# Kernel tuning notes

Hardware: AMD Instinct MI355X
Metric: run time of the kernel (lower is better)

## Reference

```python
import jax, jax.numpy as jnp
import numpy as np

E, K, H, I = 64, 8, 2048, 768  # num_experts, top_k, hidden, moe_intermediate

def setup_inputs() -> dict:
    key = jax.random.key(0)
    k1, k2, k3, k4 = jax.random.split(key, 4)
    return {
        "hidden_states": jax.random.normal(k1, (1, 1024, H), dtype=jnp.float32),
        "w_gate": jax.random.normal(k2, (H, E), dtype=jnp.float32) * 0.02,
        "w13": jax.random.normal(k3, (E, H, 2 * I), dtype=jnp.float32) * 0.02,  # fused gate+up proj
        "w2": jax.random.normal(k4, (E, I, H), dtype=jnp.float32) * 0.02,
    }

def reference(hidden_states, w_gate, w13, w2):
    orig_shape = hidden_states.shape
    x = hidden_states.reshape(-1, orig_shape[-1])            # [T, H]
    T = x.shape[0]

    # Router: logits -> softmax -> top-k -> renormalize (norm_topk_prob=True)
    router_logits = x @ w_gate                               # [T, E]
    probs = jax.nn.softmax(router_logits, axis=-1)
    topk_w, topk_idx = jax.lax.top_k(probs, K)               # [T, K]
    topk_w = topk_w / jnp.sum(topk_w, axis=-1, keepdims=True)
    # Dense combine-weight matrix [T, E] (zero for non-routed experts)
    combine = jnp.zeros((T, E), dtype=x.dtype).at[
        jnp.arange(T)[:, None], topk_idx].add(topk_w)

    # Expert SwiGLU FFN, computed densely for all experts, masked by combine
    h = jnp.einsum('th,ehd->etd', x, w13)                    # [E, T, 2I]
    gate, up = h[..., :I], h[..., I:]
    act = jax.nn.silu(gate) * up                             # [E, T, I]
    y = jnp.einsum('eti,eih->eth', act, w2)                  # [E, T, H]
    out = jnp.einsum('eth,te->th', y, combine)               # [T, H]
    return out.reshape(orig_shape)
```

## Files before the change

kernel.cpp:

```cpp
#include <hip/hip_runtime.h>
#include <hip/hip_bf16.h>
#include <math.h>

#define NE 64
#define NK 8
#define NH 2048
#define NI 768
#define NT 1024

typedef float f32x4 __attribute__((ext_vector_type(4)));
typedef __bf16 bf16x8 __attribute__((ext_vector_type(8)));
typedef __bf16 bf16x4 __attribute__((ext_vector_type(4)));

__global__ __launch_bounds__(256) void router_k(
    const float* __restrict__ x, const float* __restrict__ wg,
    __bf16* __restrict__ x_bf, int* __restrict__ topk_idx,
    float* __restrict__ topk_w, int* __restrict__ counts)
{
    __shared__ float xs[4][NH];
    const int wave = threadIdx.x >> 6;
    const int lane = threadIdx.x & 63;
    const int t = blockIdx.x * 4 + wave;

    const float* xrow = x + (size_t)t * NH;
    __bf16* brow = x_bf + (size_t)t * NH;
    #pragma unroll
    for (int j = 0; j < 8; ++j) {
        int idx = j * 256 + lane * 4;
        f32x4 v = *reinterpret_cast<const f32x4*>(xrow + idx);
        *reinterpret_cast<f32x4*>(&xs[wave][idx]) = v;
        bf16x4 b;
        b[0] = (__bf16)v.x; b[1] = (__bf16)v.y; b[2] = (__bf16)v.z; b[3] = (__bf16)v.w;
        *reinterpret_cast<bf16x4*>(brow + idx) = b;
    }
    __syncthreads();

    float a0 = 0.f, a1 = 0.f, a2 = 0.f, a3 = 0.f;
    for (int h = 0; h < NH; h += 4) {
        a0 = fmaf(xs[wave][h + 0], wg[(h + 0) * NE + lane], a0);
        a1 = fmaf(xs[wave][h + 1], wg[(h + 1) * NE + lane], a1);
        a2 = fmaf(xs[wave][h + 2], wg[(h + 2) * NE + lane], a2);
        a3 = fmaf(xs[wave][h + 3], wg[(h + 3) * NE + lane], a3);
    }
    float acc = (a0 + a1) + (a2 + a3);

    float cur = acc;
    float sel_v[NK]; int sel_i[NK];
    #pragma unroll
    for (int k = 0; k < NK; ++k) {
        float bv = cur; int bi = lane;
        #pragma unroll
        for (int s = 32; s; s >>= 1) {
            float ov = __shfl_xor(bv, s, 64);
            int   oi = __shfl_xor(bi, s, 64);
            if (ov > bv || (ov == bv && oi < bi)) { bv = ov; bi = oi; }
        }
        sel_v[k] = bv; sel_i[k] = bi;
        if (lane == bi) cur = -3.4e38f;
    }
    float m = sel_v[0];
    float ssum = 0.f;
    #pragma unroll
    for (int k = 0; k < NK; ++k) ssum += expf(sel_v[k] - m);

    if (lane < NK) {
        float w = expf(sel_v[lane] - m) / ssum;
        topk_idx[t * NK + lane] = sel_i[lane];
        topk_w[t * NK + lane] = w;
        atomicAdd(&counts[sel_i[lane]], 1);
    }
}

__global__ void scan_k(const int* __restrict__ counts, int* __restrict__ offs,
                       int* __restrict__ cursors)
{
    if (threadIdx.x == 0) {
        int r = 0;
        for (int e = 0; e < NE; ++e) { offs[e] = r; r += counts[e]; }
        offs[NE] = r;
    }
    if (threadIdx.x < NE) cursors[threadIdx.x] = 0;
}

__global__ __launch_bounds__(256) void scatter_k(
    const int* __restrict__ topk_idx, const float* __restrict__ topk_w,
    const int* __restrict__ offs, int* __restrict__ cursors,
    int* __restrict__ slot_tok, float* __restrict__ slot_w,
    int* __restrict__ slot_of)
{
    int i = blockIdx.x * 256 + threadIdx.x;
    int e = topk_idx[i];
    int p = atomicAdd(&cursors[e], 1);
    int g = offs[e] + p;
    slot_tok[g] = i >> 3;
    slot_w[g] = topk_w[i];
    slot_of[i] = g;
}

__device__ __forceinline__ int swz(int row, int ch) { return ch ^ ((row >> 1) & 3); }

__global__ __launch_bounds__(256, 2) void e1_k(
    const __bf16* __restrict__ x_bf, const float* __restrict__ w13,
    const int* __restrict__ counts, const int* __restrict__ offs,
    const int* __restrict__ slot_tok, __bf16* __restrict__ act)
{
    const int e = blockIdx.x;
    const int cnt = counts[e];
    const int m0 = blockIdx.z * 256;
    if (m0 >= cnt) return;
    const int rows = min(256, cnt - m0);
    const int n0 = blockIdx.y * 64;
    const int goff = offs[e] + m0;

    __shared__ __bf16 A[2][256 * 32];
    __shared__ __bf16 B[2][128 * 32];
    __shared__ int tok[256];

    const int tid = threadIdx.x;
    tok[tid] = (tid < rows) ? slot_tok[goff + tid] : 0;
    __syncthreads();

    const int wave = tid >> 6, lane = tid & 63;
    f32x4 acc[4][8];
    #pragma unroll
    for (int i = 0; i < 4; ++i)
        #pragma unroll
        for (int j = 0; j < 8; ++j) acc[i][j] = (f32x4){0.f, 0.f, 0.f, 0.f};

    const float* w13e = w13 + (size_t)e * NH * (2 * NI);
    const int cc = tid & 31, kch = tid >> 5;
    const int bcol0 = cc * 4;
    const int gcol = (bcol0 < 64) ? (n0 + bcol0) : (NI + n0 + bcol0 - 64);

    const __bf16* aptr[4];
    int aoff[4];
    #pragma unroll
    for (int it = 0; it < 4; ++it) {
        int item = it * 256 + tid;
        int r = item >> 2, ch = item & 3;
        aptr[it] = x_bf + (size_t)tok[r] * NH + ch * 8;
        aoff[it] = r * 32 + swz(r, ch) * 8;
    }
    const float* bptr = w13e + (size_t)(kch * 4) * (2 * NI) + gcol;
    const int lcb = kch >> 1, halfb = kch & 1;
    int boff[4];
    #pragma unroll
    for (int j = 0; j < 4; ++j)
        boff[j] = (bcol0 + j) * 32 + swz(bcol0 + j, lcb) * 8 + halfb * 4;

    bf16x8 a0v[4], a1v[4];
    f32x4 b0v[4], b1v[4];

    auto loadA = [&](bf16x8* dst, int kk) {
        #pragma unroll
        for (int it = 0; it < 4; ++it)
            dst[it] = *reinterpret_cast<const bf16x8*>(aptr[it] + kk);
    };
    auto loadB = [&](f32x4* dst, int kk) {
        #pragma unroll
        for (int ki = 0; ki < 4; ++ki)
            dst[ki] = *reinterpret_cast<const f32x4*>(bptr + (size_t)(kk + ki) * (2 * NI));
    };
    auto writeA = [&](int buf, const bf16x8* src) {
        #pragma unroll
        for (int it = 0; it < 4; ++it)
            *reinterpret_cast<bf16x8*>(&A[buf][aoff[it]]) = src[it];
    };
    auto writeB = [&](int buf, const f32x4* src) {
        #pragma unroll
        for (int j = 0; j < 4; ++j) {
            bf16x4 p;
            p[0] = (__bf16)src[0][j]; p[1] = (__bf16)src[1][j];
            p[2] = (__bf16)src[2][j]; p[3] = (__bf16)src[3][j];
            *reinterpret_cast<bf16x4*>(&B[buf][boff[j]]) = p;
        }
    };
    auto compute = [&](int buf) {
        bf16x8 bfr[8];
        #pragma unroll
        for (int nf = 0; nf < 8; ++nf) {
            int col = nf * 16 + (lane & 15);
            bfr[nf] = *reinterpret_cast<const bf16x8*>(
                &B[buf][col * 32 + swz(col, lane >> 4) * 8]);
        }
        #pragma unroll
        for (int mf = 0; mf < 4; ++mf) {
            int rf = mf * 64 + wave * 16;
            if (rf < rows) {
                int row = rf + (lane & 15);
                bf16x8 a = *reinterpret_cast<const bf16x8*>(
                    &A[buf][row * 32 + swz(row, lane >> 4) * 8]);
                #pragma unroll
                for (int nf = 0; nf < 8; ++nf)
                    acc[mf][nf] = __builtin_amdgcn_mfma_f32_16x16x32_bf16(
                        a, bfr[nf], acc[mf][nf], 0, 0, 0);
            }
        }
    };

    loadA(a0v, 0);  loadB(b0v, 0);
    loadA(a1v, 32); loadB(b1v, 32);
    writeA(0, a0v); writeB(0, b0v);
    __syncthreads();

    #pragma unroll 1
    for (int t = 0; t < 64; t += 2) {
        if (t + 2 < 64) { loadA(a0v, (t + 2) * 32); loadB(b0v, (t + 2) * 32); }
        compute(0);
        writeA(1, a1v); writeB(1, b1v);
        __syncthreads();
        if (t + 3 < 64) { loadA(a1v, (t + 3) * 32); loadB(b1v, (t + 3) * 32); }
        compute(1);
        if (t + 2 < 64) { writeA(0, a0v); writeB(0, b0v); }
        __syncthreads();
    }

    #pragma unroll
    for (int mf = 0; mf < 4; ++mf) {
        int rf = mf * 64 + wave * 16;
        if (rf >= rows) continue;
        #pragma unroll
        for (int nf = 0; nf < 4; ++nf) {
            f32x4 g = acc[mf][nf];
            f32x4 u = acc[mf][nf + 4];
            int col = n0 + nf * 16 + (lane & 15);
            #pragma unroll
            for (int r = 0; r < 4; ++r) {
                int row = rf + ((lane >> 4) << 2) + r;
                if (row < rows) {
                    float gv = g[r];
                    float a = gv / (1.f + expf(-gv)) * u[r];
                    act[(size_t)(goff + row) * NI + col] = (__bf16)a;
                }
            }
        }
    }
}

__global__ __launch_bounds__(256, 2) void e2_k(
    const __bf16* __restrict__ act, const float* __restrict__ w2,
    const int* __restrict__ counts, const int* __restrict__ offs,
    const float* __restrict__ slot_w, __bf16* __restrict__ partial)
{
    const int e = blockIdx.x;
    const int cnt = counts[e];
    const int m0 = blockIdx.z * 256;
    if (m0 >= cnt) return;
    const int rows = min(256, cnt - m0);
    const int n0 = blockIdx.y * 64;
    const int goff = offs[e] + m0;

    __shared__ __bf16 A[2][256 * 32];
    __shared__ __bf16 B[2][64 * 32];

    const int tid = threadIdx.x, wave = tid >> 6, lane = tid & 63;
    f32x4 acc[4][4];
    #pragma unroll
    for (int i = 0; i < 4; ++i)
        #pragma unroll
        for (int j = 0; j < 4; ++j) acc[i][j] = (f32x4){0.f, 0.f, 0.f, 0.f};

    const float* w2e = w2 + (size_t)e * NI * NH;
    const int cc = tid & 15, kch = (tid >> 4) & 7;
    const bool doB = tid < 128;
    const int bcol0 = cc * 4;

    const __bf16* aptr[4];
    int aoff[4];
    #pragma unroll
    for (int it = 0; it < 4; ++it) {
        int item = it * 256 + tid;
        int r = item >> 2, ch = item & 3;
        int ar = (r < rows) ? r : 0;
        aptr[it] = act + (size_t)(goff + ar) * NI + ch * 8;
        aoff[it] = r * 32 + swz(r, ch) * 8;
    }
    const float* bptr = w2e + (size_t)(kch * 4) * NH + n0 + bcol0;
    const int lcb = kch >> 1, halfb = kch & 1;
    int boff[4];
    #pragma unroll
    for (int j = 0; j < 4; ++j)
        boff[j] = (bcol0 + j) * 32 + swz(bcol0 + j, lcb) * 8 + halfb * 4;

    bf16x8 a0v[4], a1v[4];
    f32x4 b0v[4], b1v[4];

    auto loadA = [&](bf16x8* dst, int kk) {
        #pragma unroll
        for (int it = 0; it < 4; ++it)
            dst[it] = *reinterpret_cast<const bf16x8*>(aptr[it] + kk);
    };
    auto loadB = [&](f32x4* dst, int kk) {
        if (doB)
            #pragma unroll
            for (int ki = 0; ki < 4; ++ki)
                dst[ki] = *reinterpret_cast<const f32x4*>(bptr + (size_t)(kk + ki) * NH);
    };
    auto writeA = [&](int buf, const bf16x8* src) {
        #pragma unroll
        for (int it = 0; it < 4; ++it)
            *reinterpret_cast<bf16x8*>(&A[buf][aoff[it]]) = src[it];
    };
    auto writeB = [&](int buf, const f32x4* src) {
        if (doB)
            #pragma unroll
            for (int j = 0; j < 4; ++j) {
                bf16x4 p;
                p[0] = (__bf16)src[0][j]; p[1] = (__bf16)src[1][j];
                p[2] = (__bf16)src[2][j]; p[3] = (__bf16)src[3][j];
                *reinterpret_cast<bf16x4*>(&B[buf][boff[j]]) = p;
            }
    };
    auto compute = [&](int buf) {
        bf16x8 bfr[4];
        #pragma unroll
        for (int nf = 0; nf < 4; ++nf) {
            int col = nf * 16 + (lane & 15);
            bfr[nf] = *reinterpret_cast<const bf16x8*>(
                &B[buf][col * 32 + swz(col, lane >> 4) * 8]);
        }
        #pragma unroll
        for (int mf = 0; mf < 4; ++mf) {
            int rf = mf * 64 + wave * 16;
            if (rf < rows) {
                int row = rf + (lane & 15);
                bf16x8 a = *reinterpret_cast<const bf16x8*>(
                    &A[buf][row * 32 + swz(row, lane >> 4) * 8]);
                #pragma unroll
                for (int nf = 0; nf < 4; ++nf)
                    acc[mf][nf] = __builtin_amdgcn_mfma_f32_16x16x32_bf16(
                        a, bfr[nf], acc[mf][nf], 0, 0, 0);
            }
        }
    };

    loadA(a0v, 0);  loadB(b0v, 0);
    loadA(a1v, 32); loadB(b1v, 32);
    writeA(0, a0v); writeB(0, b0v);
    __syncthreads();

    #pragma unroll 1
    for (int t = 0; t < 24; t += 2) {
        if (t + 2 < 24) { loadA(a0v, (t + 2) * 32); loadB(b0v, (t + 2) * 32); }
        compute(0);
        writeA(1, a1v); writeB(1, b1v);
        __syncthreads();
        if (t + 3 < 24) { loadA(a1v, (t + 3) * 32); loadB(b1v, (t + 3) * 32); }
        compute(1);
        if (t + 2 < 24) { writeA(0, a0v); writeB(0, b0v); }
        __syncthreads();
    }

    #pragma unroll
    for (int mf = 0; mf < 4; ++mf) {
        int rf = mf * 64 + wave * 16;
        if (rf >= rows) continue;
        int rb = rf + ((lane >> 4) << 2);
        #pragma unroll
        for (int r = 0; r < 4; ++r) {
            int row = rb + r;
            if (row >= rows) continue;
            int gs = goff + row;
            float wv = slot_w[gs];
            #pragma unroll
            for (int nf = 0; nf < 4; ++nf) {
                int col = n0 + nf * 16 + (lane & 15);
                partial[(size_t)gs * NH + col] = (__bf16)(wv * acc[mf][nf][r]);
            }
        }
    }
}

__global__ __launch_bounds__(256) void combine_k(
    const __bf16* __restrict__ partial, const int* __restrict__ slot_of,
    float* __restrict__ out)
{
    const int t = blockIdx.x;
    const int c0 = threadIdx.x * 8;
    __shared__ int gs[NK];
    if (threadIdx.x < NK) gs[threadIdx.x] = slot_of[t * NK + threadIdx.x];
    __syncthreads();

    float s[8] = {0.f, 0.f, 0.f, 0.f, 0.f, 0.f, 0.f, 0.f};
    #pragma unroll
    for (int k = 0; k < NK; ++k) {
        bf16x8 v = *reinterpret_cast<const bf16x8*>(partial + (size_t)gs[k] * NH + c0);
        #pragma unroll
        for (int j = 0; j < 8; ++j) s[j] += (float)v[j];
    }
    f32x4 o0 = {s[0], s[1], s[2], s[3]};
    f32x4 o1 = {s[4], s[5], s[6], s[7]};
    *reinterpret_cast<f32x4*>(out + (size_t)t * NH + c0) = o0;
    *reinterpret_cast<f32x4*>(out + (size_t)t * NH + c0 + 4) = o1;
}

extern "C" void kernel_launch(void* const* d_in, const int* in_sizes, int n_in,
                              void* d_out, int out_size, void* d_ws, size_t ws_size,
                              hipStream_t stream)
{
    const float* x   = (const float*)d_in[0];
    const float* wg  = (const float*)d_in[1];
    const float* w13 = (const float*)d_in[2];
    const float* w2  = (const float*)d_in[3];
    float* out = (float*)d_out;
    char* ws = (char*)d_ws;

    __bf16* x_bf = (__bf16*)ws;
    size_t o = (size_t)4 * 1024 * 1024;
    __bf16* act = (__bf16*)(ws + o);      o += (size_t)8192 * NI * 2;
    __bf16* partial = (__bf16*)(ws + o);  o += (size_t)8192 * NH * 2;
    int*   topk_idx = (int*)(ws + o);     o += 8192 * 4;
    float* topk_w   = (float*)(ws + o);   o += 8192 * 4;
    int*   slot_tok = (int*)(ws + o);     o += 8192 * 4;
    float* slot_w   = (float*)(ws + o);   o += 8192 * 4;
    int*   slot_of  = (int*)(ws + o);     o += 8192 * 4;
    int*   counts   = (int*)(ws + o);     o += 256;
    int*   offs     = (int*)(ws + o);     o += 512;
    int*   cursors  = (int*)(ws + o);

    hipMemsetAsync(counts, 0, 256, stream);

    router_k <<<NT / 4, 256, 0, stream>>>(x, wg, x_bf, topk_idx, topk_w, counts);
    scan_k   <<<1, 64, 0, stream>>>(counts, offs, cursors);
    scatter_k<<<(NT * NK) / 256, 256, 0, stream>>>(topk_idx, topk_w, offs, cursors,
                                                   slot_tok, slot_w, slot_of);
    e1_k<<<dim3(NE, NI / 64, 2), 256, 0, stream>>>(x_bf, w13, counts, offs, slot_tok, act);
    e2_k<<<dim3(NE, NH / 64, 2), 256, 0, stream>>>(act, w2, counts, offs, slot_w, partial);
    combine_k<<<NT, 256, 0, stream>>>(partial, slot_of, out);
}
```

Before: 466.9 us.

## Merge scan/scatter into one kernel, pad LDS, widen e2 tiles, simplify pipeline

Merges the atomic histogram, scan and scatter into a single one-block kernel using shared-memory atomics, which removes a memset and two launches. Replaces the XOR swizzle with a padded LDS pitch of 40 and rotates B-store column order to avoid bank conflicts. Widens e2 tiles from 64 to 128 output columns so the weight loads are spread over all threads and A tiles are reused more. Reduces register prefetch from two stages to one and skips out-of-range A rows. Costs: the scatter now runs serially in one block, and e2 uses more registers and launches fewer blocks.

```diff
diff --git a/kernel.cpp b/kernel.cpp
--- a/kernel.cpp
+++ b/kernel.cpp
@@ -7,6 +7,7 @@
 #define NH 2048
 #define NI 768
 #define NT 1024
+#define APITCH 40
 
 typedef float f32x4 __attribute__((ext_vector_type(4)));
 typedef __bf16 bf16x8 __attribute__((ext_vector_type(8)));
@@ -15,7 +16,7 @@
 __global__ __launch_bounds__(256) void router_k(
     const float* __restrict__ x, const float* __restrict__ wg,
     __bf16* __restrict__ x_bf, int* __restrict__ topk_idx,
-    float* __restrict__ topk_w, int* __restrict__ counts)
+    float* __restrict__ topk_w)
 {
     __shared__ float xs[4][NH];
     const int wave = threadIdx.x >> 6;
@@ -67,37 +68,38 @@
         float w = expf(sel_v[lane] - m) / ssum;
         topk_idx[t * NK + lane] = sel_i[lane];
         topk_w[t * NK + lane] = w;
-        atomicAdd(&counts[sel_i[lane]], 1);
-    }
-}
-
-__global__ void scan_k(const int* __restrict__ counts, int* __restrict__ offs,
-                       int* __restrict__ cursors)
-{
-    if (threadIdx.x == 0) {
-        int r = 0;
-        for (int e = 0; e < NE; ++e) { offs[e] = r; r += counts[e]; }
-        offs[NE] = r;
-    }
-    if (threadIdx.x < NE) cursors[threadIdx.x] = 0;
-}
-
-__global__ __launch_bounds__(256) void scatter_k(
+    }
+}
+
+__global__ __launch_bounds__(256) void scanscatter_k(
     const int* __restrict__ topk_idx, const float* __restrict__ topk_w,
-    const int* __restrict__ offs, int* __restrict__ cursors,
+    int* __restrict__ counts, int* __restrict__ offs,
     int* __restrict__ slot_tok, float* __restrict__ slot_w,
     int* __restrict__ slot_of)
 {
-    int i = blockIdx.x * 256 + threadIdx.x;
-    int e = topk_idx[i];
-    int p = atomicAdd(&cursors[e], 1);
-    int g = offs[e] + p;
-    slot_tok[g] = i >> 3;
-    slot_w[g] = topk_w[i];
-    slot_of[i] = g;
-}
-
-__device__ __forceinline__ int swz(int row, int ch) { return ch ^ ((row >> 1) & 3); }
+    __shared__ int hist[NE], base[NE], cur[NE];
+    const int tid = threadIdx.x;
+    if (tid < NE) hist[tid] = 0;
+    __syncthreads();
+    for (int i = tid; i < NT * NK; i += 256)
+        atomicAdd(&hist[topk_idx[i]], 1);
+    __syncthreads();
+    if (tid == 0) {
+        int r = 0;
+        for (int e = 0; e < NE; ++e) { base[e] = r; r += hist[e]; }
+    }
+    __syncthreads();
+    if (tid < NE) { counts[tid] = hist[tid]; offs[tid] = base[tid]; cur[tid] = 0; }
+    __syncthreads();
+    for (int i = tid; i < NT * NK; i += 256) {
+        int e = topk_idx[i];
+        int p = atomicAdd(&cur[e], 1);
+        int g = base[e] + p;
+        slot_tok[g] = i >> 3;
+        slot_w[g] = topk_w[i];
+        slot_of[i] = g;
+    }
+}
 
 __global__ __launch_bounds__(256, 2) void e1_k(
     const __bf16* __restrict__ x_bf, const float* __restrict__ w13,
@@ -112,8 +114,8 @@
     const int n0 = blockIdx.y * 64;
     const int goff = offs[e] + m0;
 
-    __shared__ __bf16 A[2][256 * 32];
-    __shared__ __bf16 B[2][128 * 32];
+    __shared__ __bf16 A[2][256 * APITCH];
+    __shared__ __bf16 B[2][128 * APITCH];
     __shared__ int tok[256];
 
     const int tid = threadIdx.x;
@@ -131,48 +133,50 @@
     const int cc = tid & 31, kch = tid >> 5;
     const int bcol0 = cc * 4;
     const int gcol = (bcol0 < 64) ? (n0 + bcol0) : (NI + n0 + bcol0 - 64);
+    const int rot = (cc >> 1) & 3;
 
     const __bf16* aptr[4];
     int aoff[4];
+    bool aok[4];
     #pragma unroll
     for (int it = 0; it < 4; ++it) {
         int item = it * 256 + tid;
         int r = item >> 2, ch = item & 3;
         aptr[it] = x_bf + (size_t)tok[r] * NH + ch * 8;
-        aoff[it] = r * 32 + swz(r, ch) * 8;
+        aoff[it] = r * APITCH + ch * 8;
+        aok[it] = (r < rows);
     }
     const float* bptr = w13e + (size_t)(kch * 4) * (2 * NI) + gcol;
-    const int lcb = kch >> 1, halfb = kch & 1;
-    int boff[4];
-    #pragma unroll
-    for (int j = 0; j < 4; ++j)
-        boff[j] = (bcol0 + j) * 32 + swz(bcol0 + j, lcb) * 8 + halfb * 4;
-
-    bf16x8 a0v[4], a1v[4];
-    f32x4 b0v[4], b1v[4];
-
-    auto loadA = [&](bf16x8* dst, int kk) {
+    int bcol[4], boff[4];
+    #pragma unroll
+    for (int jj = 0; jj < 4; ++jj) {
+        int j = (jj + rot) & 3;
+        bcol[jj] = j;
+        boff[jj] = (bcol0 + j) * APITCH + kch * 4;
+    }
+
+    bf16x8 aReg[4];
+    f32x4 bReg[4];
+
+    auto loadT = [&](int kk) {
         #pragma unroll
         for (int it = 0; it < 4; ++it)
-            dst[it] = *reinterpret_cast<const bf16x8*>(aptr[it] + kk);
-    };
-    auto loadB = [&](f32x4* dst, int kk) {
+            if (aok[it]) aReg[it] = *reinterpret_cast<const bf16x8*>(aptr[it] + kk);
         #pragma unroll
         for (int ki = 0; ki < 4; ++ki)
-            dst[ki] = *reinterpret_cast<const f32x4*>(bptr + (size_t)(kk + ki) * (2 * NI));
-    };
-    auto writeA = [&](int buf, const bf16x8* src) {
+            bReg[ki] = *reinterpret_cast<const f32x4*>(bptr + (size_t)(kk + ki) * (2 * NI));
+    };
+    auto writeT = [&](int buf) {
         #pragma unroll
         for (int it = 0; it < 4; ++it)
-            *reinterpret_cast<bf16x8*>(&A[buf][aoff[it]]) = src[it];
-    };
-    auto writeB = [&](int buf, const f32x4* src) {
-        #pragma unroll
-        for (int j = 0; j < 4; ++j) {
+            if (aok[it]) *reinterpret_cast<bf16x8*>(&A[buf][aoff[it]]) = aReg[it];
+        #pragma unroll
+        for (int jj = 0; jj < 4; ++jj) {
+            int j = bcol[jj];
             bf16x4 p;
-            p[0] = (__bf16)src[0][j]; p[1] = (__bf16)src[1][j];
-            p[2] = (__bf16)src[2][j]; p[3] = (__bf16)src[3][j];
-            *reinterpret_cast<bf16x4*>(&B[buf][boff[j]]) = p;
+            p[0] = (__bf16)bReg[0][j]; p[1] = (__bf16)bReg[1][j];
+            p[2] = (__bf16)bReg[2][j]; p[3] = (__bf16)bReg[3][j];
+            *reinterpret_cast<bf16x4*>(&B[buf][boff[jj]]) = p;
         }
     };
     auto compute = [&](int buf) {
@@ -181,7 +185,7 @@
         for (int nf = 0; nf < 8; ++nf) {
             int col = nf * 16 + (lane & 15);
             bfr[nf] = *reinterpret_cast<const bf16x8*>(
-                &B[buf][col * 32 + swz(col, lane >> 4) * 8]);
+                &B[buf][col * APITCH + (lane >> 4) * 8]);
         }
         #pragma unroll
         for (int mf = 0; mf < 4; ++mf) {
@@ -189,7 +193,7 @@
             if (rf < rows) {
                 int row = rf + (lane & 15);
                 bf16x8 a = *reinterpret_cast<const bf16x8*>(
-                    &A[buf][row * 32 + swz(row, lane >> 4) * 8]);
+                    &A[buf][row * APITCH + (lane >> 4) * 8]);
                 #pragma unroll
                 for (int nf = 0; nf < 8; ++nf)
                     acc[mf][nf] = __builtin_amdgcn_mfma_f32_16x16x32_bf16(
@@ -198,20 +202,15 @@
         }
     };
 
-    loadA(a0v, 0);  loadB(b0v, 0);
-    loadA(a1v, 32); loadB(b1v, 32);
-    writeA(0, a0v); writeB(0, b0v);
+    loadT(0);
+    writeT(0);
     __syncthreads();
 
     #pragma unroll 1
-    for (int t = 0; t < 64; t += 2) {
-        if (t + 2 < 64) { loadA(a0v, (t + 2) * 32); loadB(b0v, (t + 2) * 32); }
-        compute(0);
-        writeA(1, a1v); writeB(1, b1v);
-        __syncthreads();
-        if (t + 3 < 64) { loadA(a1v, (t + 3) * 32); loadB(b1v, (t + 3) * 32); }
-        compute(1);
-        if (t + 2 < 64) { writeA(0, a0v); writeB(0, b0v); }
+    for (int t = 0; t < 64; ++t) {
+        if (t + 1 < 64) loadT((t + 1) * 32);
+        compute(t & 1);
+        if (t + 1 < 64) writeT((t + 1) & 1);
         __syncthreads();
     }
 
@@ -247,77 +246,75 @@
     const int m0 = blockIdx.z * 256;
     if (m0 >= cnt) return;
     const int rows = min(256, cnt - m0);
-    const int n0 = blockIdx.y * 64;
+    const int n0 = blockIdx.y * 128;
     const int goff = offs[e] + m0;
 
-    __shared__ __bf16 A[2][256 * 32];
-    __shared__ __bf16 B[2][64 * 32];
+    __shared__ __bf16 A[2][256 * APITCH];
+    __shared__ __bf16 B[2][128 * APITCH];
 
     const int tid = threadIdx.x, wave = tid >> 6, lane = tid & 63;
-    f32x4 acc[4][4];
+    f32x4 acc[4][8];
     #pragma unroll
     for (int i = 0; i < 4; ++i)
         #pragma unroll
-        for (int j = 0; j < 4; ++j) acc[i][j] = (f32x4){0.f, 0.f, 0.f, 0.f};
+        for (int j = 0; j < 8; ++j) acc[i][j] = (f32x4){0.f, 0.f, 0.f, 0.f};
 
     const float* w2e = w2 + (size_t)e * NI * NH;
-    const int cc = tid & 15, kch = (tid >> 4) & 7;
-    const bool doB = tid < 128;
+    const int cc = tid & 31, kch = tid >> 5;
     const int bcol0 = cc * 4;
+    const int rot = (cc >> 1) & 3;
 
     const __bf16* aptr[4];
     int aoff[4];
+    bool aok[4];
     #pragma unroll
     for (int it = 0; it < 4; ++it) {
         int item = it * 256 + tid;
         int r = item >> 2, ch = item & 3;
-        int ar = (r < rows) ? r : 0;
-        aptr[it] = act + (size_t)(goff + ar) * NI + ch * 8;
-        aoff[it] = r * 32 + swz(r, ch) * 8;
+        aptr[it] = act + (size_t)(goff + r) * NI + ch * 8;
+        aoff[it] = r * APITCH + ch * 8;
+        aok[it] = (r < rows);
     }
     const float* bptr = w2e + (size_t)(kch * 4) * NH + n0 + bcol0;
-    const int lcb = kch >> 1, halfb = kch & 1;
-    int boff[4];
-    #pragma unroll
-    for (int j = 0; j < 4; ++j)
-        boff[j] = (bcol0 + j) * 32 + swz(bcol0 + j, lcb) * 8 + halfb * 4;
-
-    bf16x8 a0v[4], a1v[4];
-    f32x4 b0v[4], b1v[4];
-
-    auto loadA = [&](bf16x8* dst, int kk) {
+    int bcol[4], boff[4];
+    #pragma unroll
+    for (int jj = 0; jj < 4; ++jj) {
+        int j = (jj + rot) & 3;
+        bcol[jj] = j;
+        boff[jj] = (bcol0 + j) * APITCH + kch * 4;
+    }
+
+    bf16x8 aReg[4];
+    f32x4 bReg[4];
+
+    auto loadT = [&](int kk) {
         #pragma unroll
         for (int it = 0; it < 4; ++it)
-            dst[it] = *reinterpret_cast<const bf16x8*>(aptr[it] + kk);
-    };
-    auto loadB = [&](f32x4* dst, int kk) {
-        if (doB)
-            #pragma unroll
-            for (int ki = 0; ki < 4; ++ki)
-                dst[ki] = *reinterpret_cast<const f32x4*>(bptr + (size_t)(kk + ki) * NH);
-    };
-    auto writeA = [&](int buf, const bf16x8* src) {
+            if (aok[it]) aReg[it] = *reinterpret_cast<const bf16x8*>(aptr[it] + kk);
+        #pragma unroll
+        for (int ki = 0; ki < 4; ++ki)
+            bReg[ki] = *reinterpret_cast<const f32x4*>(bptr + (size_t)(kk + ki) * NH);
+    };
+    auto writeT = [&](int buf) {
         #pragma unroll
         for (int it = 0; it < 4; ++it)
-            *reinterpret_cast<bf16x8*>(&A[buf][aoff[it]]) = src[it];
-    };
-    auto writeB = [&](int buf, const f32x4* src) {
-        if (doB)
-            #pragma unroll
-            for (int j = 0; j < 4; ++j) {
-                bf16x4 p;
-                p[0] = (__bf16)src[0][j]; p[1] = (__bf16)src[1][j];
-                p[2] = (__bf16)src[2][j]; p[3] = (__bf16)src[3][j];
-                *reinterpret_cast<bf16x4*>(&B[buf][boff[j]]) = p;
-            }
+            if (aok[it]) *reinterpret_cast<bf16x8*>(&A[buf][aoff[it]]) = aReg[it];
+        #pragma unroll
+        for (int jj = 0; jj < 4; ++jj) {
+            int j = bcol[jj];
+            bf16x4 p;
+            p[0] = (__bf16)bReg[0][j]; p[1] = (__bf16)bReg[1][j];
+            p[2] = (__bf16)bReg[2][j]; p[3] = (__bf16)bReg[3][j];
+            *reinterpret_cast<bf16x4*>(&B[buf][boff[jj]]) = p;
+        }
     };
     auto compute = [&](int buf) {
-        bf16x8 bfr[4];
-        #pragma unroll
-        for (int nf = 0; nf < 4; ++nf) {
+        bf16x8 bfr[8];
+        #pragma unroll
+        for (int nf = 0; nf < 8; ++nf) {
             int col = nf * 16 + (lane & 15);
             bfr[nf] = *reinterpret_cast<const bf16x8*>(
-                &B[buf][col * 32 + swz(col, lane >> 4) * 8]);
+                &B[buf][col * APITCH + (lane >> 4) * 8]);
         }
         #pragma unroll
         for (int mf = 0; mf < 4; ++mf) {
@@ -325,29 +322,24 @@
             if (rf < rows) {
                 int row = rf + (lane & 15);
                 bf16x8 a = *reinterpret_cast<const bf16x8*>(
-                    &A[buf][row * 32 + swz(row, lane >> 4) * 8]);
+                    &A[buf][row * APITCH + (lane >> 4) * 8]);
                 #pragma unroll
-                for (int nf = 0; nf < 4; ++nf)
+                for (int nf = 0; nf < 8; ++nf)
                     acc[mf][nf] = __builtin_amdgcn_mfma_f32_16x16x32_bf16(
                         a, bfr[nf], acc[mf][nf], 0, 0, 0);
             }
         }
     };
 
-    loadA(a0v, 0);  loadB(b0v, 0);
-    loadA(a1v, 32); loadB(b1v, 32);
-    writeA(0, a0v); writeB(0, b0v);
+    loadT(0);
+    writeT(0);
     __syncthreads();
 
     #pragma unroll 1
-    for (int t = 0; t < 24; t += 2) {
-        if (t + 2 < 24) { loadA(a0v, (t + 2) * 32); loadB(b0v, (t + 2) * 32); }
-        compute(0);
-        writeA(1, a1v); writeB(1, b1v);
-        __syncthreads();
-        if (t + 3 < 24) { loadA(a1v, (t + 3) * 32); loadB(b1v, (t + 3) * 32); }
-        compute(1);
-        if (t + 2 < 24) { writeA(0, a0v); writeB(0, b0v); }
+    for (int t = 0; t < 24; ++t) {
+        if (t + 1 < 24) loadT((t + 1) * 32);
+        compute(t & 1);
+        if (t + 1 < 24) writeT((t + 1) & 1);
         __syncthreads();
     }
 
@@ -363,7 +355,7 @@
             int gs = goff + row;
             float wv = slot_w[gs];
             #pragma unroll
-            for (int nf = 0; nf < 4; ++nf) {
+            for (int nf = 0; nf < 8; ++nf) {
                 int col = n0 + nf * 16 + (lane & 15);
                 partial[(size_t)gs * NH + col] = (__bf16)(wv * acc[mf][nf][r]);
             }
@@ -415,16 +407,12 @@
     float* slot_w   = (float*)(ws + o);   o += 8192 * 4;
     int*   slot_of  = (int*)(ws + o);     o += 8192 * 4;
     int*   counts   = (int*)(ws + o);     o += 256;
-    int*   offs     = (int*)(ws + o);     o += 512;
-    int*   cursors  = (int*)(ws + o);
-
-    hipMemsetAsync(counts, 0, 256, stream);
-
-    router_k <<<NT / 4, 256, 0, stream>>>(x, wg, x_bf, topk_idx, topk_w, counts);
-    scan_k   <<<1, 64, 0, stream>>>(counts, offs, cursors);
-    scatter_k<<<(NT * NK) / 256, 256, 0, stream>>>(topk_idx, topk_w, offs, cursors,
-                                                   slot_tok, slot_w, slot_of);
+    int*   offs     = (int*)(ws + o);     o += 256;
+
+    router_k    <<<NT / 4, 256, 0, stream>>>(x, wg, x_bf, topk_idx, topk_w);
+    scanscatter_k<<<1, 256, 0, stream>>>(topk_idx, topk_w, counts, offs,
+                                         slot_tok, slot_w, slot_of);
     e1_k<<<dim3(NE, NI / 64, 2), 256, 0, stream>>>(x_bf, w13, counts, offs, slot_tok, act);
-    e2_k<<<dim3(NE, NH / 64, 2), 256, 0, stream>>>(act, w2, counts, offs, slot_w, partial);
+    e2_k<<<dim3(NE, NH / 128, 2), 256, 0, stream>>>(act, w2, counts, offs, slot_w, partial);
     combine_k<<<NT, 256, 0, stream>>>(partial, slot_of, out);
 }
```

After: 438.4 us. -6.1%, faster.
